# Performance work log

Measured on AMD Instinct MI355X. Metric: run time of the kernel, lower is better.

Reference implementation:

```python
import jax, jax.numpy as jnp
import numpy as np

B, S, H, NH, D = 8, 512, 1024, 16, 64
SCALE = float(np.sqrt(D))

def _linear_params(key, name, d_in, d_out):
    k1, k2 = jax.random.split(key)
    lim = 1.0 / np.sqrt(d_in)
    W = jax.random.uniform(k1, (d_out, d_in), jnp.float32, -lim, lim)
    b = jax.random.uniform(k2, (d_out,), jnp.float32, -lim, lim)
    return W, b

def setup_inputs() -> dict:
    key = jax.random.key(0)
    ks = jax.random.split(key, 16)
    inp = {
        'query_states': jax.random.normal(ks[0], (B, S, H), jnp.float32),
        'key_states': jax.random.normal(ks[1], (B, S, H), jnp.float32),
        'value_states': jax.random.normal(ks[2], (B, S, H), jnp.float32),
        'attention_mask': jnp.zeros((B, 1, S, S), jnp.float32),
        'position_embedding': jax.random.normal(ks[3], (B, S, H), jnp.float32),
        'feat_embedding': jax.random.normal(ks[4], (B, S, H), jnp.float32),
    }
    names = ['q', 'k', 'v', 'qp', 'kp', 'qf', 'kf', 'd']
    for i, n in enumerate(names):
        W, b = _linear_params(ks[5 + i], n, H, H)
        inp['W' + n] = W
        inp['b' + n] = b
    return inp

def _heads(x):
    # [B,S,H] -> [B,NH,S,D]
    return x.reshape(B, S, NH, D).transpose(0, 2, 1, 3)

def _lin(x, W, b):
    return jnp.einsum('bsh,oh->bso', x, W) + b

def reference(query_states, key_states, value_states, attention_mask,
              position_embedding, feat_embedding,
              Wq, bq, Wk, bk, Wv, bv, Wqp, bqp, Wkp, bkp,
              Wqf, bqf, Wkf, bkf, Wd, bd):
    q = _heads(_lin(query_states, Wq, bq))
    k = _heads(_lin(key_states, Wk, bk))
    v = _heads(_lin(value_states, Wv, bv))
    qp = _heads(_lin(position_embedding, Wqp, bqp))
    kp = _heads(_lin(position_embedding, Wkp, bkp))
    qf = _heads(_lin(feat_embedding, Wqf, bqf))
    kf = _heads(_lin(feat_embedding, Wkf, bkf))

    attention_map = jnp.einsum('bhqd,bhkd->bhqk', q, k)        # content scores
    pos_map = jnp.einsum('bhqd,bhkd->bhqk', qp, kp)             # position scores
    feat_map = jnp.einsum('bhqd,bhkd->bhqk', qf, kf)            # feature scores

    scores = (attention_map + pos_map + feat_map) / SCALE + attention_mask
    probs = jax.nn.softmax(scores, axis=-1)
    ctx = jnp.einsum('bhqk,bhkd->bhqd', probs, v)
    ctx = ctx.transpose(0, 2, 1, 3).reshape(B, S, H)
    hidden_states = jnp.einsum('bsh,oh->bso', ctx, Wd) + bd
    return hidden_states, attention_map
```

## Files before the change

kernel.cpp:

```cpp
#include <hip/hip_runtime.h>

#define B_  8
#define S_  512
#define H_  1024
#define NH_ 16
#define D_  64
#define M_  4096
#define HH_ ((size_t)H_ * H_)
#define MH_ ((size_t)M_ * H_)

typedef __attribute__((ext_vector_type(8))) short short8;
typedef __attribute__((ext_vector_type(4))) float f32x4;

__device__ __forceinline__ unsigned short f2bf(float f) {
    unsigned u = __float_as_uint(f);
    return (unsigned short)((u + 0x7fffu + ((u >> 16) & 1u)) >> 16);
}
__device__ __forceinline__ void gload_lds16(const void* g, void* l) {
    __builtin_amdgcn_global_load_lds(
        (const __attribute__((address_space(1))) void*)g,
        (__attribute__((address_space(3))) void*)l, 16, 0, 0);
}

struct CvtArgs { const float* src[28]; unsigned short* dst[28]; };

__global__ __launch_bounds__(256) void cvt_kernel(CvtArgs a) {
    const int seg = blockIdx.y;
    const float* s = a.src[seg];
    unsigned short* d = a.dst[seg];
    const size_t i = ((size_t)blockIdx.x * 256 + threadIdx.x) * 4;
    float4 f = *(const float4*)(s + i);
    union { unsigned long long v; unsigned short h[4]; } pk;
    pk.h[0] = f2bf(f.x); pk.h[1] = f2bf(f.y);
    pk.h[2] = f2bf(f.z); pk.h[3] = f2bf(f.w);
    *(unsigned long long*)(d + i) = pk.v;
}

struct GemmPtrs { const unsigned short* x; const unsigned short* w;
                  const float* bias; void* o; };
struct GemmArgs { GemmPtrs p[7]; };

template <bool OUT_BF16>
__global__ __launch_bounds__(256) void mfma_gemm(GemmArgs args, int nwg) {
    const int dd  = blockIdx.x;
    const int cpx = nwg >> 3;
    const int l   = (dd & 7) * cpx + (dd >> 3);
    const int bz  = l >> 8;
    const int rem = l & 255;
    const int by  = rem >> 3, bx = rem & 7;
    const GemmPtrs gp = args.p[bz];

    __shared__ unsigned short As[2][128 * 32];
    __shared__ unsigned short Bs[2][128 * 32];

    const int tid  = threadIdx.x;
    const int wave = tid >> 6, lane = tid & 63;
    const int row0 = by * 128, col0 = bx * 128;
    const int wr = (wave & 1) * 64, wc = (wave >> 1) * 64;
    const int lr = lane & 15;

    const int br1 = tid >> 2,      bq1 = (tid & 3) ^ ((br1 >> 1) & 3);
    const int p2  = tid + 256;
    const int br2 = p2 >> 2,       bq2 = (p2 & 3) ^ ((br2 >> 1) & 3);

    const unsigned short* ap1 = gp.x + (size_t)(row0 + br1) * H_ + bq1 * 8;
    const unsigned short* ap2 = gp.x + (size_t)(row0 + br2) * H_ + bq2 * 8;
    const unsigned short* wp1 = gp.w + (size_t)(col0 + br1) * H_ + bq1 * 8;
    const unsigned short* wp2 = gp.w + (size_t)(col0 + br2) * H_ + bq2 * 8;

    const int slot8 = (((lane >> 4) ^ ((lr >> 1) & 3)) << 3);

    f32x4 acc[4][4];
#pragma unroll
    for (int mi = 0; mi < 4; ++mi)
#pragma unroll
        for (int ni = 0; ni < 4; ++ni) acc[mi][ni] = (f32x4)0.f;

    gload_lds16(ap1, As[0] + tid * 8);
    gload_lds16(ap2, As[0] + (tid + 256) * 8);
    gload_lds16(wp1, Bs[0] + tid * 8);
    gload_lds16(wp2, Bs[0] + (tid + 256) * 8);
    __syncthreads();

    int cur = 0;
    for (int t = 0; t < 32; ++t) {
        if (t < 31) {
            const int k1 = (t + 1) * 32;
            gload_lds16(ap1 + k1, As[cur ^ 1] + tid * 8);
            gload_lds16(ap2 + k1, As[cur ^ 1] + (tid + 256) * 8);
            gload_lds16(wp1 + k1, Bs[cur ^ 1] + tid * 8);
            gload_lds16(wp2 + k1, Bs[cur ^ 1] + (tid + 256) * 8);
        }

        const unsigned short* Ab = As[cur];
        const unsigned short* Bb = Bs[cur];
        short8 af[4], bfr[4];
#pragma unroll
        for (int mi = 0; mi < 4; ++mi)
            af[mi] = *(const short8*)(Ab + (wr + mi * 16 + lr) * 32 + slot8);
#pragma unroll
        for (int ni = 0; ni < 4; ++ni)
            bfr[ni] = *(const short8*)(Bb + (wc + ni * 16 + lr) * 32 + slot8);
#pragma unroll
        for (int mi = 0; mi < 4; ++mi)
#pragma unroll
            for (int ni = 0; ni < 4; ++ni)
                acc[mi][ni] = __builtin_amdgcn_mfma_f32_16x16x32_bf16(
                    af[mi], bfr[ni], acc[mi][ni], 0, 0, 0);

        __syncthreads();
        cur ^= 1;
    }

    float bv[4];
#pragma unroll
    for (int ni = 0; ni < 4; ++ni)
        bv[ni] = gp.bias[col0 + wc + ni * 16 + lr];

#pragma unroll
    for (int mi = 0; mi < 4; ++mi)
#pragma unroll
        for (int r = 0; r < 4; ++r) {
            const int row = row0 + wr + mi * 16 + (lane >> 4) * 4 + r;
#pragma unroll
            for (int ni = 0; ni < 4; ++ni) {
                const int col = col0 + wc + ni * 16 + lr;
                const float v = acc[mi][ni][r] + bv[ni];
                if (OUT_BF16)
                    ((unsigned short*)gp.o)[(size_t)row * H_ + col] = f2bf(v);
                else
                    ((float*)gp.o)[(size_t)row * H_ + col] = v;
            }
        }
}

__global__ __launch_bounds__(256) void attn_kernel(
        const unsigned short* __restrict__ ws,
        const float* __restrict__ mask,
        float* __restrict__ amap,
        unsigned short* __restrict__ ctxo) {
    const unsigned short* qm0 = ws;
    const unsigned short* qm1 = ws + 3 * MH_;
    const unsigned short* qm2 = ws + 5 * MH_;
    const unsigned short* km0 = ws + 1 * MH_;
    const unsigned short* km1 = ws + 4 * MH_;
    const unsigned short* km2 = ws + 6 * MH_;
    const unsigned short* vm  = ws + 2 * MH_;

    __shared__ unsigned short Ks[3][64 * 64];
    __shared__ unsigned short Vt[64 * 64];
    __shared__ unsigned short Ps[4][16 * 64];

    const int blk = blockIdx.x;
    const int l   = (blk & 7) * 128 + (blk >> 3);
    const int qt  = l & 7;
    const int bh  = l >> 3;
    const int b   = bh >> 4, h = bh & 15;
    const int tid = threadIdx.x;
    const int w   = tid >> 6, lane = tid & 63;
    const int lr  = lane & 15, g = lane >> 4;

    short8 qc[2], qp_[2], qf_[2];
    {
        const int qrow = qt * 64 + w * 16 + lr;
        const size_t base = ((size_t)(b * S_) + qrow) * H_ + h * D_ + g * 8;
#pragma unroll
        for (int kc = 0; kc < 2; ++kc) {
            qc[kc]  = *(const short8*)(qm0 + base + kc * 32);
            qp_[kc] = *(const short8*)(qm1 + base + kc * 32);
            qf_[kc] = *(const short8*)(qm2 + base + kc * 32);
        }
    }

    const int p1 = tid,        r1 = p1 >> 3, s1 = (p1 & 7) ^ (r1 & 7);
    const int p2 = tid + 256,  r2 = p2 >> 3, s2 = (p2 & 7) ^ (r2 & 7);
    const size_t kb1 = ((size_t)(b * S_) + r1) * H_ + h * D_ + s1 * 8;
    const size_t kb2 = ((size_t)(b * S_) + r2) * H_ + h * D_ + s2 * 8;
    unsigned short* kd1[3] = { Ks[0] + p1 * 8, Ks[1] + p1 * 8, Ks[2] + p1 * 8 };
    unsigned short* kd2[3] = { Ks[0] + p2 * 8, Ks[1] + p2 * 8, Ks[2] + p2 * 8 };
    const unsigned short* ksrc[3] = { km0, km1, km2 };

    const int vk  = (tid & 31) * 2;
    const int vdg = tid >> 5;
    const unsigned short* vp0 = vm + ((size_t)(b * S_) + vk) * H_ + h * D_ + vdg * 8;

    const int soffA = ((0 + g) ^ (lr & 7)) * 8;
    const int soffB = ((4 + g) ^ (lr & 7)) * 8;

    f32x4 oacc[4];
    float mrun[4], lrun[4];
#pragma unroll
    for (int i = 0; i < 4; ++i) {
        oacc[i] = (f32x4)0.f; mrun[i] = -1e30f; lrun[i] = 0.f;
    }

    for (int t = 0; t < 8; ++t) {
        const size_t koff = (size_t)(t * 64) * H_;
        __syncthreads();

        union { uint4 u; unsigned short h[8]; } va, vb;
        va.u = *(const uint4*)(vp0 + koff);
        vb.u = *(const uint4*)(vp0 + koff + H_);

#pragma unroll
        for (int m = 0; m < 3; ++m) {
            gload_lds16(ksrc[m] + kb1 + koff, kd1[m]);
            gload_lds16(ksrc[m] + kb2 + koff, kd2[m]);
        }

#pragma unroll
        for (int j = 0; j < 8; ++j) {
            const int d = vdg * 8 + j;
            const unsigned pk = (unsigned)va.h[j] | ((unsigned)vb.h[j] << 16);
            *(unsigned*)(Vt + d * 64 + (((vk >> 3) ^ (d & 7)) * 8) + (vk & 7)) = pk;
        }
        __syncthreads();

        f32x4 accC[4], accS[4];
#pragma unroll
        for (int ni = 0; ni < 4; ++ni) { accC[ni] = (f32x4)0.f; accS[ni] = (f32x4)0.f; }
#pragma unroll
        for (int ni = 0; ni < 4; ++ni) {
            const int rowb = (ni * 16 + lr) * 64;
            short8 c0 = *(const short8*)(Ks[0] + rowb + soffA);
            short8 c1 = *(const short8*)(Ks[0] + rowb + soffB);
            short8 p0 = *(const short8*)(Ks[1] + rowb + soffA);
            short8 p1f = *(const short8*)(Ks[1] + rowb + soffB);
            short8 f0 = *(const short8*)(Ks[2] + rowb + soffA);
            short8 f1 = *(const short8*)(Ks[2] + rowb + soffB);
            accC[ni] = __builtin_amdgcn_mfma_f32_16x16x32_bf16(qc[0], c0, accC[ni], 0, 0, 0);
            accC[ni] = __builtin_amdgcn_mfma_f32_16x16x32_bf16(qc[1], c1, accC[ni], 0, 0, 0);
            accS[ni] = __builtin_amdgcn_mfma_f32_16x16x32_bf16(qp_[0], p0, accS[ni], 0, 0, 0);
            accS[ni] = __builtin_amdgcn_mfma_f32_16x16x32_bf16(qp_[1], p1f, accS[ni], 0, 0, 0);
            accS[ni] = __builtin_amdgcn_mfma_f32_16x16x32_bf16(qf_[0], f0, accS[ni], 0, 0, 0);
            accS[ni] = __builtin_amdgcn_mfma_f32_16x16x32_bf16(qf_[1], f1, accS[ni], 0, 0, 0);
        }

        const int key0 = t * 64;
        float st[4][4];
#pragma unroll
        for (int ni = 0; ni < 4; ++ni) {
            const int col = key0 + ni * 16 + lr;
#pragma unroll
            for (int r = 0; r < 4; ++r) {
                const int row = qt * 64 + w * 16 + g * 4 + r;
                amap[((size_t)bh * S_ + row) * S_ + col] = accC[ni][r];
                const float mval =
                    mask[(size_t)b * S_ * S_ + (size_t)row * S_ + col];
                st[ni][r] = (accC[ni][r] + accS[ni][r]) * 0.125f + mval;
            }
        }

#pragma unroll
        for (int r = 0; r < 4; ++r) {
            float tmax = fmaxf(fmaxf(st[0][r], st[1][r]),
                               fmaxf(st[2][r], st[3][r]));
#pragma unroll
            for (int off = 8; off >= 1; off >>= 1)
                tmax = fmaxf(tmax, __shfl_xor(tmax, off));
            const float mnew = fmaxf(mrun[r], tmax);
            const float e0 = __expf(st[0][r] - mnew);
            const float e1 = __expf(st[1][r] - mnew);
            const float e2 = __expf(st[2][r] - mnew);
            const float e3 = __expf(st[3][r] - mnew);
            float esum = (e0 + e1) + (e2 + e3);
#pragma unroll
            for (int off = 8; off >= 1; off >>= 1)
                esum += __shfl_xor(esum, off);
            const float alpha = __expf(mrun[r] - mnew);
            lrun[r] = lrun[r] * alpha + esum;
            mrun[r] = mnew;
#pragma unroll
            for (int nd = 0; nd < 4; ++nd) oacc[nd][r] *= alpha;

            const int prow = g * 4 + r;
            unsigned short* pb = Ps[w] + prow * 64;
            const int sw = prow & 7, lh = lr >> 3, lw = lr & 7;
            pb[((0 + lh) ^ sw) * 8 + lw] = f2bf(e0);
            pb[((2 + lh) ^ sw) * 8 + lw] = f2bf(e1);
            pb[((4 + lh) ^ sw) * 8 + lw] = f2bf(e2);
            pb[((6 + lh) ^ sw) * 8 + lw] = f2bf(e3);
        }

#pragma unroll
        for (int kc = 0; kc < 2; ++kc) {
            const int soff = kc ? soffB : soffA;
            short8 pa = *(const short8*)(Ps[w] + lr * 64 + soff);
#pragma unroll
            for (int nd = 0; nd < 4; ++nd) {
                short8 vb2 = *(const short8*)(Vt + (nd * 16 + lr) * 64 + soff);
                oacc[nd] = __builtin_amdgcn_mfma_f32_16x16x32_bf16(
                    pa, vb2, oacc[nd], 0, 0, 0);
            }
        }
    }

#pragma unroll
    for (int r = 0; r < 4; ++r) {
        const float inv = 1.0f / lrun[r];
        const int row = qt * 64 + w * 16 + g * 4 + r;
#pragma unroll
        for (int nd = 0; nd < 4; ++nd)
            ctxo[((size_t)(b * S_) + row) * H_ + h * D_ + nd * 16 + lr] =
                f2bf(oacc[nd][r] * inv);
    }
}

extern "C" void kernel_launch(void* const* d_in, const int* in_sizes, int n_in,
                              void* d_out, int out_size, void* d_ws, size_t ws_size,
                              hipStream_t stream) {
    const float* in[22];
    for (int i = 0; i < 22; ++i) in[i] = (const float*)d_in[i];

    unsigned short* wsW = (unsigned short*)d_ws;
    unsigned short* wsP = wsW + 8 * HH_;
    unsigned short* wsC = wsP + 7 * MH_;
    unsigned short* wsA = wsC + 1 * MH_;
    float*          out = (float*)d_out;

    CvtArgs ca;
    {
        int ci = 0;
        const int widx[8] = { 6, 8, 10, 12, 14, 16, 18, 20 };
        for (int i = 0; i < 8; ++i, ++ci) {
            ca.src[ci] = in[widx[i]];
            ca.dst[ci] = wsW + i * HH_;
        }
        const int aidx[5] = { 0, 1, 2, 4, 5 };
        for (int i = 0; i < 5; ++i)
            for (int c = 0; c < 4; ++c, ++ci) {
                ca.src[ci] = in[aidx[i]] + (size_t)c * HH_;
                ca.dst[ci] = wsA + i * MH_ + (size_t)c * HH_;
            }
    }
    cvt_kernel<<<dim3(1024, 28), 256, 0, stream>>>(ca);

    GemmArgs ga;
    ga.p[0] = { wsA + 0 * MH_, wsW + 0 * HH_, in[7],  wsP + 0 * MH_ };
    ga.p[1] = { wsA + 1 * MH_, wsW + 1 * HH_, in[9],  wsP + 1 * MH_ };
    ga.p[2] = { wsA + 2 * MH_, wsW + 2 * HH_, in[11], wsP + 2 * MH_ };
    ga.p[3] = { wsA + 3 * MH_, wsW + 3 * HH_, in[13], wsP + 3 * MH_ };
    ga.p[4] = { wsA + 3 * MH_, wsW + 4 * HH_, in[15], wsP + 4 * MH_ };
    ga.p[5] = { wsA + 4 * MH_, wsW + 5 * HH_, in[17], wsP + 5 * MH_ };
    ga.p[6] = { wsA + 4 * MH_, wsW + 6 * HH_, in[19], wsP + 6 * MH_ };
    mfma_gemm<true><<<dim3(1792), 256, 0, stream>>>(ga, 1792);

    attn_kernel<<<dim3(1024), 256, 0, stream>>>(wsP, in[3], out + MH_, wsC);

    GemmArgs gf;
    gf.p[0] = { wsC, wsW + 7 * HH_, in[21], out };
    for (int i = 1; i < 7; ++i) gf.p[i] = gf.p[0];
    mfma_gemm<false><<<dim3(256), 256, 0, stream>>>(gf, 256);
}
```

Measured before the change: 428.4 us.

## Deepen GEMM LDS pipeline to four stages with counted vmcnt waits

The projection GEMM moves from a double-buffered LDS pipeline to a 4-buffer ring that keeps three K-tiles of global-to-LDS loads in flight. Per-iteration __syncthreads is replaced by explicit s_waitcnt vmcnt counts plus a raw s_barrier, so the block only waits for the oldest tile. The loop is fully unrolled and the MFMA block is wrapped in s_setprio. LDS use doubles, to 64KB per block, which may reduce occupancy, and the hand-counted waits rely on the compiler not reordering the global_load_lds instructions.

Result: faster. 407.5 us (-4.9%).

```diff
diff --git a/kernel.cpp b/kernel.cpp
--- a/kernel.cpp
+++ b/kernel.cpp
@@ -50,8 +50,8 @@
     const int by  = rem >> 3, bx = rem & 7;
     const GemmPtrs gp = args.p[bz];
 
-    __shared__ unsigned short As[2][128 * 32];
-    __shared__ unsigned short Bs[2][128 * 32];
+    __shared__ unsigned short As[4][128 * 32];
+    __shared__ unsigned short Bs[4][128 * 32];
 
     const int tid  = threadIdx.x;
     const int wave = tid >> 6, lane = tid & 63;
@@ -76,24 +76,22 @@
 #pragma unroll
         for (int ni = 0; ni < 4; ++ni) acc[mi][ni] = (f32x4)0.f;
 
-    gload_lds16(ap1, As[0] + tid * 8);
-    gload_lds16(ap2, As[0] + (tid + 256) * 8);
-    gload_lds16(wp1, Bs[0] + tid * 8);
-    gload_lds16(wp2, Bs[0] + (tid + 256) * 8);
-    __syncthreads();
-
-    int cur = 0;
+#pragma unroll
+    for (int pt = 0; pt < 3; ++pt) {
+        const int kk = pt * 32;
+        gload_lds16(ap1 + kk, As[pt] + tid * 8);
+        gload_lds16(ap2 + kk, As[pt] + (tid + 256) * 8);
+        gload_lds16(wp1 + kk, Bs[pt] + tid * 8);
+        gload_lds16(wp2 + kk, Bs[pt] + (tid + 256) * 8);
+    }
+    asm volatile("s_waitcnt vmcnt(8)" ::: "memory");
+    __builtin_amdgcn_sched_barrier(0);
+    __builtin_amdgcn_s_barrier();
+
+#pragma unroll
     for (int t = 0; t < 32; ++t) {
-        if (t < 31) {
-            const int k1 = (t + 1) * 32;
-            gload_lds16(ap1 + k1, As[cur ^ 1] + tid * 8);
-            gload_lds16(ap2 + k1, As[cur ^ 1] + (tid + 256) * 8);
-            gload_lds16(wp1 + k1, Bs[cur ^ 1] + tid * 8);
-            gload_lds16(wp2 + k1, Bs[cur ^ 1] + (tid + 256) * 8);
-        }
-
-        const unsigned short* Ab = As[cur];
-        const unsigned short* Bb = Bs[cur];
+        const unsigned short* Ab = As[t & 3];
+        const unsigned short* Bb = Bs[t & 3];
         short8 af[4], bfr[4];
 #pragma unroll
         for (int mi = 0; mi < 4; ++mi)
@@ -101,15 +99,32 @@
 #pragma unroll
         for (int ni = 0; ni < 4; ++ni)
             bfr[ni] = *(const short8*)(Bb + (wc + ni * 16 + lr) * 32 + slot8);
+
+        if (t + 3 < 32) {
+            const int kk = (t + 3) * 32;
+            const int s  = (t + 3) & 3;
+            gload_lds16(ap1 + kk, As[s] + tid * 8);
+            gload_lds16(ap2 + kk, As[s] + (tid + 256) * 8);
+            gload_lds16(wp1 + kk, Bs[s] + tid * 8);
+            gload_lds16(wp2 + kk, Bs[s] + (tid + 256) * 8);
+        }
+
+        __builtin_amdgcn_s_setprio(1);
 #pragma unroll
         for (int mi = 0; mi < 4; ++mi)
 #pragma unroll
             for (int ni = 0; ni < 4; ++ni)
                 acc[mi][ni] = __builtin_amdgcn_mfma_f32_16x16x32_bf16(
                     af[mi], bfr[ni], acc[mi][ni], 0, 0, 0);
-
-        __syncthreads();
-        cur ^= 1;
+        __builtin_amdgcn_s_setprio(0);
+
+        if (t < 29)       asm volatile("s_waitcnt vmcnt(8)" ::: "memory");
+        else if (t == 29) asm volatile("s_waitcnt vmcnt(4)" ::: "memory");
+        else if (t == 30) asm volatile("s_waitcnt vmcnt(0)" ::: "memory");
+        if (t < 31) {
+            __builtin_amdgcn_sched_barrier(0);
+            __builtin_amdgcn_s_barrier();
+        }
     }
 
     float bv[4];
```

## Load GEMM weight fragments directly into registers instead of staging through LDS

Applied to the files above, without the earlier changes.

The B (weight) operand no longer goes through shared memory. Each lane loads its MFMA fragment straight from global memory into a double-buffered register array, one step ahead. This removes half of the LDS traffic and LDS capacity, and the K loop is fully unrolled with s_setprio raised around the MFMA block. The cost is that the weights are no longer shared between the two waves that use the same columns, so global and L2 traffic for the weights doubles. Register pressure also rises from the extra fragments and the unrolled loop.

New measurement: 469.3 us. +9.5%, slower.

```diff
diff --git a/kernel.cpp b/kernel.cpp
--- a/kernel.cpp
+++ b/kernel.cpp
@@ -51,13 +51,12 @@
     const GemmPtrs gp = args.p[bz];
 
     __shared__ unsigned short As[2][128 * 32];
-    __shared__ unsigned short Bs[2][128 * 32];
 
     const int tid  = threadIdx.x;
     const int wave = tid >> 6, lane = tid & 63;
     const int row0 = by * 128, col0 = bx * 128;
     const int wr = (wave & 1) * 64, wc = (wave >> 1) * 64;
-    const int lr = lane & 15;
+    const int lr = lane & 15, g = lane >> 4;
 
     const int br1 = tid >> 2,      bq1 = (tid & 3) ^ ((br1 >> 1) & 3);
     const int p2  = tid + 256;
@@ -65,10 +64,13 @@
 
     const unsigned short* ap1 = gp.x + (size_t)(row0 + br1) * H_ + bq1 * 8;
     const unsigned short* ap2 = gp.x + (size_t)(row0 + br2) * H_ + bq2 * 8;
-    const unsigned short* wp1 = gp.w + (size_t)(col0 + br1) * H_ + bq1 * 8;
-    const unsigned short* wp2 = gp.w + (size_t)(col0 + br2) * H_ + bq2 * 8;
-
-    const int slot8 = (((lane >> 4) ^ ((lr >> 1) & 3)) << 3);
+
+    const unsigned short* wb[4];
+#pragma unroll
+    for (int ni = 0; ni < 4; ++ni)
+        wb[ni] = gp.w + (size_t)(col0 + wc + ni * 16 + lr) * H_ + g * 8;
+
+    const int slot8 = ((g ^ ((lr >> 1) & 3)) << 3);
 
     f32x4 acc[4][4];
 #pragma unroll
@@ -78,38 +80,39 @@
 
     gload_lds16(ap1, As[0] + tid * 8);
     gload_lds16(ap2, As[0] + (tid + 256) * 8);
-    gload_lds16(wp1, Bs[0] + tid * 8);
-    gload_lds16(wp2, Bs[0] + (tid + 256) * 8);
+    short8 breg[2][4];
+#pragma unroll
+    for (int ni = 0; ni < 4; ++ni)
+        breg[0][ni] = *(const short8*)(wb[ni]);
     __syncthreads();
 
-    int cur = 0;
+#pragma unroll
     for (int t = 0; t < 32; ++t) {
         if (t < 31) {
-            const int k1 = (t + 1) * 32;
-            gload_lds16(ap1 + k1, As[cur ^ 1] + tid * 8);
-            gload_lds16(ap2 + k1, As[cur ^ 1] + (tid + 256) * 8);
-            gload_lds16(wp1 + k1, Bs[cur ^ 1] + tid * 8);
-            gload_lds16(wp2 + k1, Bs[cur ^ 1] + (tid + 256) * 8);
-        }
-
-        const unsigned short* Ab = As[cur];
-        const unsigned short* Bb = Bs[cur];
-        short8 af[4], bfr[4];
+            const int kk = (t + 1) * 32;
+            gload_lds16(ap1 + kk, As[(t + 1) & 1] + tid * 8);
+            gload_lds16(ap2 + kk, As[(t + 1) & 1] + (tid + 256) * 8);
+#pragma unroll
+            for (int ni = 0; ni < 4; ++ni)
+                breg[(t + 1) & 1][ni] = *(const short8*)(wb[ni] + kk);
+        }
+
+        const unsigned short* Ab = As[t & 1];
+        short8 af[4];
 #pragma unroll
         for (int mi = 0; mi < 4; ++mi)
             af[mi] = *(const short8*)(Ab + (wr + mi * 16 + lr) * 32 + slot8);
-#pragma unroll
-        for (int ni = 0; ni < 4; ++ni)
-            bfr[ni] = *(const short8*)(Bb + (wc + ni * 16 + lr) * 32 + slot8);
+
+        __builtin_amdgcn_s_setprio(1);
 #pragma unroll
         for (int mi = 0; mi < 4; ++mi)
 #pragma unroll
             for (int ni = 0; ni < 4; ++ni)
                 acc[mi][ni] = __builtin_amdgcn_mfma_f32_16x16x32_bf16(
-                    af[mi], bfr[ni], acc[mi][ni], 0, 0, 0);
-
-        __syncthreads();
-        cur ^= 1;
+                    af[mi], breg[t & 1][ni], acc[mi][ni], 0, 0, 0);
+        __builtin_amdgcn_s_setprio(0);
+
+        if (t < 31) __syncthreads();
     }
 
     float bv[4];
```
